# Kernel optimization log

Hardware: AMD Instinct MI355X
Metric: run time of the kernel (lower is better)

Reference implementation:

```python
import jax, jax.numpy as jnp
import numpy as np

B, S, HID = 1, 4096, 2048
NH, NKV, HD, RD = 16, 4, 128, 64
EPS = 1e-6
SCALE = HD ** -0.5


def _rmsnorm(x, w, eps=EPS):
    x32 = x.astype(jnp.float32)
    var = jnp.mean(x32 * x32, axis=-1, keepdims=True)
    return (w * (x32 * jax.lax.rsqrt(var + eps))).astype(x.dtype)


def _rotate_half(x):
    x1, x2 = jnp.split(x, 2, axis=-1)
    return jnp.concatenate([-x2, x1], axis=-1)


def setup_inputs() -> dict:
    key = jax.random.key(0)
    ks = jax.random.split(key, 6)
    hidden_states = jax.random.normal(ks[0], (B, S, HID), dtype=jnp.float32)
    # real rotary embeddings for rotary_dim=RD
    inv_freq = 1.0 / (10000.0 ** (jnp.arange(0, RD, 2, dtype=jnp.float32) / RD))
    pos = jnp.arange(S, dtype=jnp.float32)
    freqs = pos[:, None] * inv_freq[None, :]          # [S, RD/2]
    emb = jnp.concatenate([freqs, freqs], axis=-1)     # [S, RD]
    cos = jnp.cos(emb)[None]                           # [1, S, RD]
    sin = jnp.sin(emb)[None]
    w = 0.02
    Wq = jax.random.normal(ks[1], (NH * HD, HID), dtype=jnp.float32) * w
    Wk = jax.random.normal(ks[2], (NKV * HD, HID), dtype=jnp.float32) * w
    Wv = jax.random.normal(ks[3], (NKV * HD, HID), dtype=jnp.float32) * w
    Wo = jax.random.normal(ks[4], (HID, NH * HD), dtype=jnp.float32) * w
    q_norm_w = jnp.ones((NH * HD,), dtype=jnp.float32)
    k_norm_w = jnp.ones((NKV * HD,), dtype=jnp.float32)
    return {"hidden_states": hidden_states, "cos": cos, "sin": sin,
            "Wq": Wq, "Wk": Wk, "Wv": Wv, "Wo": Wo,
            "q_norm_w": q_norm_w, "k_norm_w": k_norm_w}


def _attention(hidden_states, cos, sin, Wq, Wk, Wv, Wo, q_norm_w, k_norm_w):
    bsz, q_len, _ = hidden_states.shape
    q = hidden_states @ Wq.T                 # [B,S,NH*HD]
    k = hidden_states @ Wk.T                 # [B,S,NKV*HD]
    v = hidden_states @ Wv.T
    q = _rmsnorm(q, q_norm_w)
    k = _rmsnorm(k, k_norm_w)
    q = q.reshape(bsz, q_len, NH, HD).transpose(0, 2, 1, 3)   # b h s d
    k = k.reshape(bsz, q_len, NKV, HD).transpose(0, 2, 1, 3)
    v = v.reshape(bsz, q_len, NKV, HD).transpose(0, 2, 1, 3)
    # partial RoPE on first RD dims
    c = cos[:, None]  # [B,1,S,RD]
    s = sin[:, None]
    q_rot, q_pass = q[..., :RD], q[..., RD:]
    k_rot, k_pass = k[..., :RD], k[..., RD:]
    q = jnp.concatenate([q_rot * c + _rotate_half(q_rot) * s, q_pass], axis=-1)
    k = jnp.concatenate([k_rot * c + _rotate_half(k_rot) * s, k_pass], axis=-1)
    # GQA: repeat kv heads
    n_rep = NH // NKV
    k = jnp.repeat(k, n_rep, axis=1)
    v = jnp.repeat(v, n_rep, axis=1)
    scores = jnp.einsum('bhqd,bhkd->bhqk', q, k) * SCALE
    causal = jnp.triu(jnp.full((q_len, q_len), -jnp.inf, dtype=scores.dtype), k=1)
    scores = scores + causal
    probs = jax.nn.softmax(scores.astype(jnp.float32), axis=-1).astype(q.dtype)
    out = jnp.einsum('bhqk,bhkd->bhqd', probs, v)
    out = out.transpose(0, 2, 1, 3).reshape(bsz, q_len, NH * HD)
    return out @ Wo.T


def reference(hidden_states, cos, sin, Wq, Wk, Wv, Wo, q_norm_w, k_norm_w):
    return _attention(hidden_states, cos, sin, Wq, Wk, Wv, Wo, q_norm_w, k_norm_w)
```

## Files before the change

kernel.cpp:

```cpp
#include <hip/hip_runtime.h>

typedef unsigned short u16;
typedef unsigned int   u32;
typedef __bf16 bf16x8 __attribute__((ext_vector_type(8)));
typedef float  f32x4  __attribute__((ext_vector_type(4)));

#define S_LEN 4096
#define HIDN  2048
#define NHEAD 16
#define NKVH  4
#define HDIM  128
#define ROTD  64
#define QKVN  3072

__device__ __forceinline__ u16 f2bf(float f) {
  union { float f; u32 u; } v; v.f = f;
  u32 r = v.u + 0x7FFFu + ((v.u >> 16) & 1u);
  return (u16)(r >> 16);
}
__device__ __forceinline__ u16 f2bf_fast(float f) {
  union { __bf16 b; u16 u; } cv; cv.b = (__bf16)f; return cv.u;
}
__device__ __forceinline__ float bf2f(u16 u) {
  union { u32 u; float f; } v; v.u = ((u32)u) << 16; return v.f;
}
__device__ __forceinline__ void gl2lds16(const u16* g, u16* l) {
  __builtin_amdgcn_global_load_lds((const __attribute__((address_space(1))) void*)g,
                                   (__attribute__((address_space(3))) void*)l, 16, 0, 0);
}
__device__ __forceinline__ f32x4 mfma_bf16(bf16x8 a, bf16x8 b, f32x4 c) {
  return __builtin_amdgcn_mfma_f32_16x16x32_bf16(a, b, c, 0, 0, 0);
}
template <int N> __device__ __forceinline__ void vmwait() {
  if constexpr (N == 7)      asm volatile("s_waitcnt vmcnt(7)" ::: "memory");
  else if constexpr (N == 6) asm volatile("s_waitcnt vmcnt(6)" ::: "memory");
  else                       asm volatile("s_waitcnt vmcnt(0)" ::: "memory");
}

__global__ __launch_bounds__(256) void cvt_f32_bf16(const float* __restrict__ in,
                                                    u16* __restrict__ out) {
  size_t i = ((size_t)blockIdx.x * 256 + threadIdx.x) * 8;
  float4 a = *(const float4*)(in + i);
  float4 b = *(const float4*)(in + i + 4);
  uint4 r;
  r.x = (u32)f2bf(a.x) | ((u32)f2bf(a.y) << 16);
  r.y = (u32)f2bf(a.z) | ((u32)f2bf(a.w) << 16);
  r.z = (u32)f2bf(b.x) | ((u32)f2bf(b.y) << 16);
  r.w = (u32)f2bf(b.z) | ((u32)f2bf(b.w) << 16);
  *(uint4*)(out + i) = r;
}

template <int BN, int NB, bool BF16OUT>
__global__ __launch_bounds__(512, 2) void gemm_big(const u16* __restrict__ A,
                                                   const u16* __restrict__ Bm,
                                                   void* __restrict__ Cp,
                                                   int M, int N, int K) {
  constexpr int WNC = BN / 4;
  constexpr int NF  = WNC / 16;
  constexpr int ASZ = 256 * 128;
  constexpr int BUF = ASZ + BN * 128;
  constexpr int LOADS = 4 + NB;
  __shared__ __align__(1024) char lds[2 * BUF];

  const int tid = threadIdx.x, wave = tid >> 6, lane = tid & 63;
  const int wm = wave >> 2, wn = wave & 3;
  const int row0 = blockIdx.x * 256, col0 = blockIdx.y * BN;
  const int l8 = lane >> 3, l7 = lane & 7;
  const int T = K >> 6;

  const u16* gA[4]; const u16* gB[NB];
  u16* ldsA[4]; u16* ldsB[NB];
  #pragma unroll
  for (int i = 0; i < 4; ++i) {
    gA[i]  = A + (size_t)(row0 + wave * 32 + i * 8 + l8) * K + (l7 ^ l8) * 8;
    ldsA[i] = (u16*)(lds + wave * 4096 + i * 1024);
  }
  #pragma unroll
  for (int i = 0; i < NB; ++i) {
    gB[i]  = Bm + (size_t)(col0 + wave * (BN / 8) + i * 8 + l8) * K + (l7 ^ l8) * 8;
    ldsB[i] = (u16*)(lds + ASZ + wave * (BN * 16) + i * 1024);
  }
  auto stage = [&](int buf, int t) {
    const size_t ko = (size_t)t * 64;
    #pragma unroll
    for (int i = 0; i < 4; ++i)
      gl2lds16(gA[i] + ko, (u16*)((char*)ldsA[i] + buf * BUF));
    #pragma unroll
    for (int i = 0; i < NB; ++i)
      gl2lds16(gB[i] + ko, (u16*)((char*)ldsB[i] + buf * BUF));
  };

  const int colx0 = (((lane >> 4))     ^ l7) * 16;
  const int colx1 = ((4 + (lane >> 4)) ^ l7) * 16;
  const char* aB = lds + (wm * 128 + (lane & 15)) * 128;
  const char* bB = lds + ASZ + (wn * WNC + (lane & 15)) * 128;

  f32x4 acc[8][NF];
  #pragma unroll
  for (int i = 0; i < 8; ++i)
    #pragma unroll
    for (int j = 0; j < NF; ++j) { f32x4 z = {0.f,0.f,0.f,0.f}; acc[i][j] = z; }

  stage(0, 0);
  stage(1, 1);
  vmwait<LOADS>();
  __builtin_amdgcn_s_barrier();

  for (int t = 0; t < T; ++t) {
    const int bo = (t & 1) * BUF;
    #pragma unroll
    for (int kh = 0; kh < 2; ++kh) {
      const int cx = kh ? colx1 : colx0;
      bf16x8 bfr[NF];
      #pragma unroll
      for (int nf = 0; nf < NF; ++nf)
        bfr[nf] = *(const bf16x8*)(bB + bo + nf * 2048 + cx);
      #pragma unroll
      for (int mh = 0; mh < 2; ++mh) {
        bf16x8 af[4];
        #pragma unroll
        for (int mf = 0; mf < 4; ++mf)
          af[mf] = *(const bf16x8*)(aB + bo + mh * 8192 + mf * 2048 + cx);
        __builtin_amdgcn_s_setprio(1);
        #pragma unroll
        for (int mf = 0; mf < 4; ++mf)
          #pragma unroll
          for (int nf = 0; nf < NF; ++nf)
            acc[mh * 4 + mf][nf] = mfma_bf16(af[mf], bfr[nf], acc[mh * 4 + mf][nf]);
        __builtin_amdgcn_s_setprio(0);
      }
    }
    asm volatile("s_waitcnt lgkmcnt(0)" ::: "memory");
    __builtin_amdgcn_s_barrier();
    if (t + 2 < T) stage(t & 1, t + 2);
    if (t + 1 < T) {
      if (t + 2 < T) vmwait<LOADS>();
      else           vmwait<0>();
      __builtin_amdgcn_s_barrier();
    }
  }

  const int mwv = row0 + wm * 128, nwv = col0 + wn * WNC;
  #pragma unroll
  for (int mf8 = 0; mf8 < 8; ++mf8)
    #pragma unroll
    for (int nf = 0; nf < NF; ++nf)
      #pragma unroll
      for (int r = 0; r < 4; ++r) {
        int m = mwv + (mf8 >> 2) * 64 + (mf8 & 3) * 16 + (lane >> 4) * 4 + r;
        int n = nwv + nf * 16 + (lane & 15);
        float v = acc[mf8][nf][r];
        if (BF16OUT) ((u16*)Cp)[(size_t)m * N + n] = f2bf(v);
        else         ((float*)Cp)[(size_t)m * N + n] = v;
      }
}

__global__ __launch_bounds__(256) void norm_rope(const u16* __restrict__ qkv,
                                                 const float* __restrict__ cosb,
                                                 const float* __restrict__ sinb,
                                                 const float* __restrict__ qw,
                                                 const float* __restrict__ kw,
                                                 u16* __restrict__ Qo,
                                                 u16* __restrict__ Ko) {
  const int s = blockIdx.x, t = threadIdx.x;
  const int wave = t >> 6, lane = t & 63;
  const float SL = 0.08838834764831845f * 1.4426950408889634f;
  __shared__ float rowbuf[HIDN];
  __shared__ float red[4];
  const u16* base = qkv + (size_t)s * QKVN;

  float x[8];
  {
    uint4 v = *(const uint4*)(base + t * 8);
    u32 w4[4] = {v.x, v.y, v.z, v.w};
    #pragma unroll
    for (int j = 0; j < 4; ++j) {
      x[2*j]   = bf2f((u16)(w4[j] & 0xffffu));
      x[2*j+1] = bf2f((u16)(w4[j] >> 16));
    }
  }
  float ss = 0.f;
  #pragma unroll
  for (int j = 0; j < 8; ++j) ss += x[j] * x[j];
  #pragma unroll
  for (int m = 1; m < 64; m <<= 1) ss += __shfl_xor(ss, m);
  if (lane == 0) red[wave] = ss;
  __syncthreads();
  float rs = rsqrtf((red[0]+red[1]+red[2]+red[3]) * (1.0f / HIDN) + 1e-6f);
  #pragma unroll
  for (int j = 0; j < 8; ++j) rowbuf[t*8 + j] = x[j] * rs * qw[t*8 + j];
  __syncthreads();
  {
    int i0 = t * 8, d0 = i0 & (HDIM - 1), hh = i0 >> 7;
    float o[8];
    if (d0 < ROTD) {
      #pragma unroll
      for (int j = 0; j < 8; ++j) {
        int d = d0 + j;
        float rot = (d < 32) ? -rowbuf[i0 + j + 32] : rowbuf[i0 + j - 32];
        o[j] = rowbuf[i0 + j] * cosb[s*ROTD + d] + rot * sinb[s*ROTD + d];
      }
    } else {
      #pragma unroll
      for (int j = 0; j < 8; ++j) o[j] = rowbuf[i0 + j];
    }
    uint4 r;
    r.x = (u32)f2bf(o[0]*SL) | ((u32)f2bf(o[1]*SL) << 16);
    r.y = (u32)f2bf(o[2]*SL) | ((u32)f2bf(o[3]*SL) << 16);
    r.z = (u32)f2bf(o[4]*SL) | ((u32)f2bf(o[5]*SL) << 16);
    r.w = (u32)f2bf(o[6]*SL) | ((u32)f2bf(o[7]*SL) << 16);
    *(uint4*)(Qo + ((size_t)hh * S_LEN + s) * HDIM + d0) = r;
  }

  const u16* kbase = base + HIDN;
  float y0, y1;
  { u32 v = *(const u32*)(kbase + t * 2); y0 = bf2f((u16)(v & 0xffffu)); y1 = bf2f((u16)(v >> 16)); }
  float ss2 = y0*y0 + y1*y1;
  #pragma unroll
  for (int m = 1; m < 64; m <<= 1) ss2 += __shfl_xor(ss2, m);
  __syncthreads();
  if (lane == 0) red[wave] = ss2;
  __syncthreads();
  float rs2 = rsqrtf((red[0]+red[1]+red[2]+red[3]) * (1.0f / 512.0f) + 1e-6f);
  rowbuf[t*2]     = y0 * rs2 * kw[t*2];
  rowbuf[t*2 + 1] = y1 * rs2 * kw[t*2 + 1];
  __syncthreads();
  {
    int i0 = t * 2, d0 = i0 & (HDIM - 1), hh = i0 >> 7;
    float o0, o1;
    if (d0 < ROTD) {
      float r0 = (d0 < 32) ? -rowbuf[i0 + 32] : rowbuf[i0 - 32];
      float r1 = (d0 + 1 < 32) ? -rowbuf[i0 + 1 + 32] : rowbuf[i0 + 1 - 32];
      o0 = rowbuf[i0]     * cosb[s*ROTD + d0]     + r0 * sinb[s*ROTD + d0];
      o1 = rowbuf[i0 + 1] * cosb[s*ROTD + d0 + 1] + r1 * sinb[s*ROTD + d0 + 1];
    } else { o0 = rowbuf[i0]; o1 = rowbuf[i0 + 1]; }
    u32 r = (u32)f2bf(o0) | ((u32)f2bf(o1) << 16);
    *(u32*)(Ko + ((size_t)hh * S_LEN + s) * HDIM + d0) = r;
  }
}

__global__ __launch_bounds__(256) void vtrans(const u16* __restrict__ qkv,
                                              u16* __restrict__ Vt) {
  const int sb = blockIdx.x * 64, db = blockIdx.y * 64, kvh = blockIdx.z;
  __shared__ u16 tile[64][72];
  const int t = threadIdx.x;
  {
    int r = t >> 2, cc = (t & 3) * 16;
    const u16* src = qkv + (size_t)(sb + r) * QKVN + 2560 + kvh * HDIM + db + cc;
    *(uint4*)&tile[r][cc]     = *(const uint4*)(src);
    *(uint4*)&tile[r][cc + 8] = *(const uint4*)(src + 8);
  }
  __syncthreads();
  {
    int d = t >> 2, sc = (t & 3) * 16;
    u16 tmp[16];
    #pragma unroll
    for (int j = 0; j < 16; ++j) tmp[j] = tile[sc + j][d];
    u16* dst = Vt + ((size_t)kvh * HDIM + db + d) * S_LEN + sb + sc;
    *(uint4*)dst       = *(uint4*)&tmp[0];
    *(uint4*)(dst + 8) = *(uint4*)&tmp[8];
  }
}

__global__ __launch_bounds__(256, 2) void attn_fwd(const u16* __restrict__ Q,
                                                   const u16* __restrict__ K,
                                                   const u16* __restrict__ Vt,
                                                   u16* __restrict__ O) {
  const int n    = blockIdx.x;
  const int slot = n & 7, kq = n >> 3;
  const int kvh  = slot >> 1;
  const int h    = kvh * 4 + (slot & 1) * 2 + (kq & 1);
  const int p    = kq >> 1;
  const int tid = threadIdx.x, wave = tid >> 6, lane = tid & 63;
  __shared__ u16 Ks[2][64][128];
  __shared__ u16 Vs[2][128][64];
  __shared__ u16 Ps[4][16][64];

  const u16* gKb[4]; const u16* gVb[4];
  #pragma unroll
  for (int i = 0; i < 4; ++i) {
    int cc = wave * 4 + i;
    int rk = cc * 4 + (lane >> 4);
    gKb[i] = K + ((size_t)kvh * S_LEN + rk) * HDIM + ((lane & 15) ^ (rk & 7)) * 8;
    int rv = cc * 8 + (lane >> 3);
    gVb[i] = Vt + ((size_t)kvh * HDIM + rv) * S_LEN + ((lane & 7) ^ (rv & 7)) * 8;
  }
  auto stage = [&](int buf, int kvb) {
    #pragma unroll
    for (int i = 0; i < 4; ++i) {
      int cc = wave * 4 + i;
      gl2lds16(gKb[i] + (size_t)kvb * HDIM, &Ks[buf][cc * 4][0]);
      gl2lds16(gVb[i] + kvb,                &Vs[buf][cc * 8][0]);
    }
  };

  int offv[4];
  #pragma unroll
  for (int kk = 0; kk < 4; ++kk)
    offv[kk] = (kk * 64 + (lane >> 4) * 16) ^ ((lane & 7) << 4);
  const char* ksB = (const char*)Ks + (lane & 15) * 256;
  const char* vsB = (const char*)Vs + (lane & 15) * 128;
  const char* psB = (const char*)Ps + wave * 2048 + (lane & 15) * 128;
  char*       pwB = (char*)Ps + wave * 2048;
  const int   lx2 = (lane & 15) * 2;

  stage(0, 0);
  __syncthreads();
  int cur = 0;

  for (int job = 0; job < 2; ++job) {
    const int qb = job ? (63 - p) : p;
    const int ntiles = qb + 1;
    const int qg = qb * 64 + wave * 16 + (lane >> 4) * 4;

    bf16x8 qf[4];
    {
      const u16* qptr = Q + ((size_t)h * S_LEN + qb * 64 + wave * 16 + (lane & 15)) * HDIM
                        + (lane >> 4) * 8;
      #pragma unroll
      for (int kk = 0; kk < 4; ++kk) qf[kk] = *(const bf16x8*)(qptr + kk * 32);
    }

    float lsum[4] = {0.f, 0.f, 0.f, 0.f};
    f32x4 o[8];
    #pragma unroll
    for (int i = 0; i < 8; ++i) { f32x4 z = {0.f,0.f,0.f,0.f}; o[i] = z; }

    for (int kt = 0; kt < ntiles; ++kt) {
      if (kt + 1 < ntiles)      stage(cur ^ 1, (kt + 1) * 64);
      else if (job == 0)        stage(cur ^ 1, 0);

      const int bufo = cur << 14;

      f32x4 sc[4];
      #pragma unroll
      for (int i = 0; i < 4; ++i) { f32x4 z = {0.f,0.f,0.f,0.f}; sc[i] = z; }
      __builtin_amdgcn_s_setprio(1);
      #pragma unroll
      for (int kk = 0; kk < 4; ++kk)
        #pragma unroll
        for (int nf = 0; nf < 4; ++nf) {
          bf16x8 kf = *(const bf16x8*)(ksB + bufo + nf * 4096 + offv[kk]);
          sc[nf] = mfma_bf16(qf[kk], kf, sc[nf]);
        }
      __builtin_amdgcn_s_setprio(0);

      if (kt == ntiles - 1) {
        const int kvb = kt * 64;
        #pragma unroll
        for (int nf = 0; nf < 4; ++nf) {
          int col = kvb + nf * 16 + (lane & 15);
          #pragma unroll
          for (int r = 0; r < 4; ++r) {
            float e = __builtin_amdgcn_exp2f(sc[nf][r]);
            e = (col <= qg + r) ? e : 0.f;
            sc[nf][r] = e;
            lsum[r] += e;
          }
        }
      } else {
        #pragma unroll
        for (int nf = 0; nf < 4; ++nf)
          #pragma unroll
          for (int r = 0; r < 4; ++r) {
            float e = __builtin_amdgcn_exp2f(sc[nf][r]);
            sc[nf][r] = e;
            lsum[r] += e;
          }
      }

      #pragma unroll
      for (int nf = 0; nf < 4; ++nf)
        #pragma unroll
        for (int r = 0; r < 4; ++r) {
          int prow = (lane >> 4) * 4 + r;
          int bcol = (nf * 32 + lx2) ^ ((prow & 7) << 4);
          *(u16*)(pwB + prow * 128 + bcol) = f2bf_fast(sc[nf][r]);
        }

      __builtin_amdgcn_s_setprio(1);
      #pragma unroll
      for (int ks = 0; ks < 2; ++ks) {
        bf16x8 pf = *(const bf16x8*)(psB + offv[ks]);
        #pragma unroll
        for (int nf2 = 0; nf2 < 8; ++nf2) {
          bf16x8 vf = *(const bf16x8*)(vsB + bufo + nf2 * 2048 + offv[ks]);
          o[nf2] = mfma_bf16(pf, vf, o[nf2]);
        }
      }
      __builtin_amdgcn_s_setprio(0);

      __syncthreads();
      cur ^= 1;
    }

    #pragma unroll
    for (int r = 0; r < 4; ++r) {
      float lt = lsum[r];
      #pragma unroll
      for (int m = 1; m < 16; m <<= 1) lt += __shfl_xor(lt, m);
      float inv = 1.f / lt;
      int srow = qg + r;
      #pragma unroll
      for (int nf2 = 0; nf2 < 8; ++nf2) {
        int col = h * HDIM + nf2 * 16 + (lane & 15);
        O[(size_t)srow * HIDN + col] = f2bf_fast(o[nf2][r] * inv);
      }
    }
  }
}

extern "C" void kernel_launch(void* const* d_in, const int* in_sizes, int n_in,
                              void* d_out, int out_size, void* d_ws, size_t ws_size,
                              hipStream_t stream) {
  (void)in_sizes; (void)n_in; (void)out_size; (void)ws_size;
  const float* h    = (const float*)d_in[0];
  const float* cosb = (const float*)d_in[1];
  const float* sinb = (const float*)d_in[2];
  const float* Wq   = (const float*)d_in[3];
  const float* Wk   = (const float*)d_in[4];
  const float* Wv   = (const float*)d_in[5];
  const float* Wo   = (const float*)d_in[6];
  const float* qw   = (const float*)d_in[7];
  const float* kw   = (const float*)d_in[8];
  float* out = (float*)d_out;

  char* ws = (char*)d_ws;
  u16* hbf  = (u16*)(ws);
  u16* Kb   = (u16*)(ws + (16u << 20));
  u16* Vtb  = (u16*)(ws + (20u << 20));
  u16* wqkv = (u16*)(ws + (24u << 20));
  u16* Qb   = (u16*)(ws + (24u << 20));
  u16* qkvb = (u16*)(ws + (40u << 20));
  u16* wob  = (u16*)(ws + (40u << 20));

  cvt_f32_bf16<<<4096, 256, 0, stream>>>(h, hbf);
  cvt_f32_bf16<<<2048, 256, 0, stream>>>(Wq, wqkv);
  cvt_f32_bf16<<<512, 256, 0, stream>>>(Wk, wqkv + 4u * 1024 * 1024);
  cvt_f32_bf16<<<512, 256, 0, stream>>>(Wv, wqkv + 5u * 1024 * 1024);

  gemm_big<192, 3, true><<<dim3(16, 16), 512, 0, stream>>>(hbf, wqkv, qkvb,
                                                           4096, 3072, 2048);

  norm_rope<<<4096, 256, 0, stream>>>(qkvb, cosb, sinb, qw, kw, Qb, Kb);
  vtrans<<<dim3(64, 2, 4), 256, 0, stream>>>(qkvb, Vtb);

  cvt_f32_bf16<<<2048, 256, 0, stream>>>(Wo, wob);

  attn_fwd<<<dim3(512), 256, 0, stream>>>(Qb, Kb, Vtb, hbf);

  gemm_big<128, 2, false><<<dim3(16, 16), 512, 0, stream>>>(hbf, wob, out,
                                                            4096, 2048, 2048);
}
```

Before: 253.0 us.

## Share K/V tiles across two heads per block with 32-row wave tiles

Each attention block now handles two query heads of the same KV group. Each wave computes 32 query rows of one head instead of 16, so every K and V fragment read from LDS feeds two MFMAs, and each staged K/V tile serves twice the query work. The grid is halved to 256 blocks, which lowers global K/V staging traffic and LDS reads per FLOP. In exchange register pressure roughly doubles for the accumulators and Q fragments, and with fewer blocks the GPU may be underfilled (256 blocks versus 256 CUs) and load balance may suffer.

```diff
diff --git a/kernel.cpp b/kernel.cpp
--- a/kernel.cpp
+++ b/kernel.cpp
@@ -266,15 +266,15 @@
                                                    const u16* __restrict__ K,
                                                    const u16* __restrict__ Vt,
                                                    u16* __restrict__ O) {
-  const int n    = blockIdx.x;
-  const int slot = n & 7, kq = n >> 3;
-  const int kvh  = slot >> 1;
-  const int h    = kvh * 4 + (slot & 1) * 2 + (kq & 1);
-  const int p    = kq >> 1;
+  const int bid  = blockIdx.x;
+  const int slot = bid & 7, p = bid >> 3;
+  const int kvh  = slot >> 1, hp = slot & 1;
   const int tid = threadIdx.x, wave = tid >> 6, lane = tid & 63;
+  const int h  = kvh * 4 + hp * 2 + (wave >> 1);
+  const int wq = wave & 1;
   __shared__ u16 Ks[2][64][128];
   __shared__ u16 Vs[2][128][64];
-  __shared__ u16 Ps[4][16][64];
+  __shared__ u16 Ps[4][32][64];
 
   const u16* gKb[4]; const u16* gVb[4];
   #pragma unroll
@@ -300,8 +300,8 @@
     offv[kk] = (kk * 64 + (lane >> 4) * 16) ^ ((lane & 7) << 4);
   const char* ksB = (const char*)Ks + (lane & 15) * 256;
   const char* vsB = (const char*)Vs + (lane & 15) * 128;
-  const char* psB = (const char*)Ps + wave * 2048 + (lane & 15) * 128;
-  char*       pwB = (char*)Ps + wave * 2048;
+  const char* psB = (const char*)Ps + wave * 4096 + (lane & 15) * 128;
+  char*       pwB = (char*)Ps + wave * 4096;
   const int   lx2 = (lane & 15) * 2;
 
   stage(0, 0);
@@ -311,20 +311,27 @@
   for (int job = 0; job < 2; ++job) {
     const int qb = job ? (63 - p) : p;
     const int ntiles = qb + 1;
-    const int qg = qb * 64 + wave * 16 + (lane >> 4) * 4;
-
-    bf16x8 qf[4];
-    {
-      const u16* qptr = Q + ((size_t)h * S_LEN + qb * 64 + wave * 16 + (lane & 15)) * HDIM
+    const int qg0 = qb * 64 + wq * 32 + (lane >> 4) * 4;
+
+    bf16x8 qf[2][4];
+    #pragma unroll
+    for (int qm = 0; qm < 2; ++qm) {
+      const u16* qptr = Q + ((size_t)h * S_LEN + qb * 64 + wq * 32 + qm * 16 + (lane & 15)) * HDIM
                         + (lane >> 4) * 8;
       #pragma unroll
-      for (int kk = 0; kk < 4; ++kk) qf[kk] = *(const bf16x8*)(qptr + kk * 32);
-    }
-
-    float lsum[4] = {0.f, 0.f, 0.f, 0.f};
-    f32x4 o[8];
-    #pragma unroll
-    for (int i = 0; i < 8; ++i) { f32x4 z = {0.f,0.f,0.f,0.f}; o[i] = z; }
+      for (int kk = 0; kk < 4; ++kk) qf[qm][kk] = *(const bf16x8*)(qptr + kk * 32);
+    }
+
+    float lsum[2][4];
+    #pragma unroll
+    for (int qm = 0; qm < 2; ++qm)
+      #pragma unroll
+      for (int r = 0; r < 4; ++r) lsum[qm][r] = 0.f;
+    f32x4 o[2][8];
+    #pragma unroll
+    for (int qm = 0; qm < 2; ++qm)
+      #pragma unroll
+      for (int i = 0; i < 8; ++i) { f32x4 z = {0.f,0.f,0.f,0.f}; o[qm][i] = z; }
 
     for (int kt = 0; kt < ntiles; ++kt) {
       if (kt + 1 < ntiles)      stage(cur ^ 1, (kt + 1) * 64);
@@ -332,60 +339,71 @@
 
       const int bufo = cur << 14;
 
-      f32x4 sc[4];
-      #pragma unroll
-      for (int i = 0; i < 4; ++i) { f32x4 z = {0.f,0.f,0.f,0.f}; sc[i] = z; }
+      f32x4 sc[2][4];
+      #pragma unroll
+      for (int qm = 0; qm < 2; ++qm)
+        #pragma unroll
+        for (int i = 0; i < 4; ++i) { f32x4 z = {0.f,0.f,0.f,0.f}; sc[qm][i] = z; }
       __builtin_amdgcn_s_setprio(1);
       #pragma unroll
       for (int kk = 0; kk < 4; ++kk)
         #pragma unroll
         for (int nf = 0; nf < 4; ++nf) {
           bf16x8 kf = *(const bf16x8*)(ksB + bufo + nf * 4096 + offv[kk]);
-          sc[nf] = mfma_bf16(qf[kk], kf, sc[nf]);
+          sc[0][nf] = mfma_bf16(qf[0][kk], kf, sc[0][nf]);
+          sc[1][nf] = mfma_bf16(qf[1][kk], kf, sc[1][nf]);
         }
       __builtin_amdgcn_s_setprio(0);
 
       if (kt == ntiles - 1) {
         const int kvb = kt * 64;
         #pragma unroll
-        for (int nf = 0; nf < 4; ++nf) {
-          int col = kvb + nf * 16 + (lane & 15);
+        for (int qm = 0; qm < 2; ++qm)
           #pragma unroll
-          for (int r = 0; r < 4; ++r) {
-            float e = __builtin_amdgcn_exp2f(sc[nf][r]);
-            e = (col <= qg + r) ? e : 0.f;
-            sc[nf][r] = e;
-            lsum[r] += e;
+          for (int nf = 0; nf < 4; ++nf) {
+            int col = kvb + nf * 16 + (lane & 15);
+            #pragma unroll
+            for (int r = 0; r < 4; ++r) {
+              float e = __builtin_amdgcn_exp2f(sc[qm][nf][r]);
+              e = (col <= qg0 + qm * 16 + r) ? e : 0.f;
+              sc[qm][nf][r] = e;
+              lsum[qm][r] += e;
+            }
           }
-        }
       } else {
+        #pragma unroll
+        for (int qm = 0; qm < 2; ++qm)
+          #pragma unroll
+          for (int nf = 0; nf < 4; ++nf)
+            #pragma unroll
+            for (int r = 0; r < 4; ++r) {
+              float e = __builtin_amdgcn_exp2f(sc[qm][nf][r]);
+              sc[qm][nf][r] = e;
+              lsum[qm][r] += e;
+            }
+      }
+
+      #pragma unroll
+      for (int qm = 0; qm < 2; ++qm)
         #pragma unroll
         for (int nf = 0; nf < 4; ++nf)
           #pragma unroll
           for (int r = 0; r < 4; ++r) {
-            float e = __builtin_amdgcn_exp2f(sc[nf][r]);
-            sc[nf][r] = e;
-            lsum[r] += e;
+            int prow = qm * 16 + (lane >> 4) * 4 + r;
+            int bcol = (nf * 32 + lx2) ^ ((prow & 7) << 4);
+            *(u16*)(pwB + prow * 128 + bcol) = f2bf_fast(sc[qm][nf][r]);
           }
-      }
-
-      #pragma unroll
-      for (int nf = 0; nf < 4; ++nf)
-        #pragma unroll
-        for (int r = 0; r < 4; ++r) {
-          int prow = (lane >> 4) * 4 + r;
-          int bcol = (nf * 32 + lx2) ^ ((prow & 7) << 4);
-          *(u16*)(pwB + prow * 128 + bcol) = f2bf_fast(sc[nf][r]);
-        }
 
       __builtin_amdgcn_s_setprio(1);
       #pragma unroll
       for (int ks = 0; ks < 2; ++ks) {
-        bf16x8 pf = *(const bf16x8*)(psB + offv[ks]);
+        bf16x8 pf0 = *(const bf16x8*)(psB + offv[ks]);
+        bf16x8 pf1 = *(const bf16x8*)(psB + 2048 + offv[ks]);
         #pragma unroll
         for (int nf2 = 0; nf2 < 8; ++nf2) {
           bf16x8 vf = *(const bf16x8*)(vsB + bufo + nf2 * 2048 + offv[ks]);
-          o[nf2] = mfma_bf16(pf, vf, o[nf2]);
+          o[0][nf2] = mfma_bf16(pf0, vf, o[0][nf2]);
+          o[1][nf2] = mfma_bf16(pf1, vf, o[1][nf2]);
         }
       }
       __builtin_amdgcn_s_setprio(0);
@@ -395,18 +413,20 @@
     }
 
     #pragma unroll
-    for (int r = 0; r < 4; ++r) {
-      float lt = lsum[r];
-      #pragma unroll
-      for (int m = 1; m < 16; m <<= 1) lt += __shfl_xor(lt, m);
-      float inv = 1.f / lt;
-      int srow = qg + r;
-      #pragma unroll
-      for (int nf2 = 0; nf2 < 8; ++nf2) {
-        int col = h * HDIM + nf2 * 16 + (lane & 15);
-        O[(size_t)srow * HIDN + col] = f2bf_fast(o[nf2][r] * inv);
-      }
-    }
+    for (int qm = 0; qm < 2; ++qm)
+      #pragma unroll
+      for (int r = 0; r < 4; ++r) {
+        float lt = lsum[qm][r];
+        #pragma unroll
+        for (int m = 1; m < 16; m <<= 1) lt += __shfl_xor(lt, m);
+        float inv = 1.f / lt;
+        int srow = qg0 + qm * 16 + r;
+        #pragma unroll
+        for (int nf2 = 0; nf2 < 8; ++nf2) {
+          int col = h * HDIM + nf2 * 16 + (lane & 15);
+          O[(size_t)srow * HIDN + col] = f2bf_fast(o[qm][nf2][r] * inv);
+        }
+      }
   }
 }
 
@@ -447,7 +467,7 @@
 
   cvt_f32_bf16<<<2048, 256, 0, stream>>>(Wo, wob);
 
-  attn_fwd<<<dim3(512), 256, 0, stream>>>(Qb, Kb, Vtb, hbf);
+  attn_fwd<<<dim3(256), 256, 0, stream>>>(Qb, Kb, Vtb, hbf);
 
   gemm_big<128, 2, false><<<dim3(16, 16), 512, 0, stream>>>(hbf, wob, out,
                                                             4096, 2048, 2048);
```

After: 267.0 us, median of 2. 1.06x slower.
